# Kernel optimization log

Measured on AMD Instinct MI355X. Metric: run time of the kernel, lower is better.

The kernel has to match this reference:

```python
import jax, jax.numpy as jnp
import numpy as np

H = 50  # hidden_size


def _lstm_layer(x_seq, W_ih, W_hh, b):
    """Single-layer LSTM over a full sequence.
    x_seq: [B, T, D]; W_ih: [4H, D]; W_hh: [4H, H]; b: [4H] (b_ih + b_hh).
    Gate order matches PyTorch: i, f, g, o. Returns hidden seq [B, T, H].
    """
    B = x_seq.shape[0]
    # Precompute the input projection for every timestep in one GEMM.
    xW = jnp.einsum('btd,gd->btg', x_seq, W_ih) + b          # [B, T, 4H]
    xW = jnp.swapaxes(xW, 0, 1)                              # [T, B, 4H] time-major for scan

    def step(carry, xg):
        h, c = carry
        gates = xg + h @ W_hh.T                              # [B, 4H]
        i, f, g, o = jnp.split(gates, 4, axis=-1)
        i = jax.nn.sigmoid(i)
        f = jax.nn.sigmoid(f)
        g = jnp.tanh(g)
        o = jax.nn.sigmoid(o)
        c = f * c + i * g
        h = o * jnp.tanh(c)
        return (h, c), h

    init = (jnp.zeros((B, H), x_seq.dtype), jnp.zeros((B, H), x_seq.dtype))
    _, hs = jax.lax.scan(step, init, xW)                     # hs: [T, B, H]
    return jnp.swapaxes(hs, 0, 1)                            # [B, T, H]


def setup_inputs() -> dict:
    key = jax.random.key(0)
    ks = jax.random.split(key, 9)
    B, T, D, O = 4096, 512, 2, 1
    s = 1.0 / np.sqrt(H)  # PyTorch LSTM init scale: U(-1/sqrt(H), 1/sqrt(H))
    u = lambda k, shape: jax.random.uniform(k, shape, jnp.float32, -s, s)
    return {
        'x': jax.random.normal(ks[0], (B, T, D), jnp.float32),
        'W_ih0': u(ks[1], (4 * H, D)),
        'W_hh0': u(ks[2], (4 * H, H)),
        'b0': u(ks[3], (4 * H,)),   # b_ih + b_hh folded into one bias (identical math)
        'W_ih1': u(ks[4], (4 * H, H)),
        'W_hh1': u(ks[5], (4 * H, H)),
        'b1': u(ks[6], (4 * H,)),
        'W_fc': u(ks[7], (O, H)),
        'b_fc': u(ks[8], (O,)),
    }


def reference(x, W_ih0, W_hh0, b0, W_ih1, W_hh1, b1, W_fc, b_fc):
    h0 = _lstm_layer(x, W_ih0, W_hh0, b0)    # [B, T, H] layer 0
    h1 = _lstm_layer(h0, W_ih1, W_hh1, b1)   # [B, T, H] layer 1
    # Final-step linear head: out = fc(out[:, -1, :])
    return h1[:, -1, :] @ W_fc.T + b_fc      # [B, 1]
```

## Files before the change

### kernel.cpp

```cpp
#include <hip/hip_runtime.h>


typedef _Float16 f16;
typedef f16  f16x8 __attribute__((ext_vector_type(8)));
typedef float f32x4 __attribute__((ext_vector_type(4)));
typedef unsigned short u16;
typedef unsigned int   u32;

#define TT   512
#define MB   16
#define KP   136
#define XTP  513
#define BLK  512

__device__ __forceinline__ float sigm(float x) {
    return __builtin_amdgcn_rcpf(1.0f + __expf(-x));
}
__device__ __forceinline__ float tanh_(float x) {
    return 1.0f - 2.0f * __builtin_amdgcn_rcpf(__expf(2.0f * x) + 1.0f);
}

__device__ __forceinline__ float welem(int layer, int g, int u, int k,
        const float* __restrict__ Wih0, const float* __restrict__ Whh0,
        const float* __restrict__ b0,
        const float* __restrict__ Wih1, const float* __restrict__ Whh1,
        const float* __restrict__ b1) {
    if (u >= 50) return 0.0f;
    const int row = g * 50 + u;
    if (layer == 0) {
        if (k < 50)  return Whh0[row * 50 + k];
        if (k < 52)  return Wih0[row * 2 + (k - 50)];
        if (k == 52) return b0[row];
        return 0.0f;
    } else {
        if (k < 50)             return Wih1[row * 50 + k];
        if (k == 52)            return b1[row];
        if (k >= 64 && k < 114) return Whh1[row * 50 + (k - 64)];
        return 0.0f;
    }
}

extern "C" __global__ void __launch_bounds__(BLK, 2)
lstm2_mfma8(const float* __restrict__ x,
            const float* __restrict__ W_ih0, const float* __restrict__ W_hh0,
            const float* __restrict__ b0,
            const float* __restrict__ W_ih1, const float* __restrict__ W_hh1,
            const float* __restrict__ b1,
            const float* __restrict__ W_fc,  const float* __restrict__ b_fc,
            float* __restrict__ out)
{
    __shared__ __align__(16) u16 hc[2][MB][KP];
    __shared__ u32  xpack[MB][XTP];
    __shared__ float hfin[MB][52];

    const int tid   = threadIdx.x;
    const int lane  = tid & 63;
    const int wid   = tid >> 6;
    const int layer = wid >> 2;
    const int ub    = wid & 3;
    const int col   = lane & 15;
    const int kg    = lane >> 4;
    const int bbase = blockIdx.x * MB;

    for (int idx = tid; idx < MB * TT; idx += BLK) {
        const int b = idx >> 9, t = idx & (TT - 1);
        const float2 v = *reinterpret_cast<const float2*>(
            x + ((size_t)(bbase + b) * TT + t) * 2);
        xpack[b][t] = (u32)__builtin_bit_cast(u16, (f16)v.x)
                    | ((u32)__builtin_bit_cast(u16, (f16)v.y) << 16);
    }
    {
        u32* hcU = reinterpret_cast<u32*>(&hc[0][0][0]);
        for (int i = tid; i < 2 * MB * KP / 2; i += BLK) hcU[i] = 0;
    }
    __syncthreads();
    if (tid < 32) hc[tid >> 4][tid & 15][52] = (u16)0x3C00;
    else if (tid < 48)
        *reinterpret_cast<u32*>(&hc[0][tid - 32][50]) = xpack[tid - 32][0];

    const int u = 16 * ub + col;
    f16x8 bf[4][4];
#pragma unroll
    for (int g = 0; g < 4; ++g) {
#pragma unroll
        for (int kf = 0; kf < 4; ++kf) {
            f16x8 v;
#pragma unroll
            for (int e = 0; e < 8; ++e)
                v[e] = (f16)welem(layer, g, u, kf * 32 + 8 * kg + e,
                                  W_ih0, W_hh0, b0, W_ih1, W_hh1, b1);
            bf[g][kf] = v;
        }
    }

    float cst[4] = {0.f, 0.f, 0.f, 0.f};
    __syncthreads();

    for (int it = 0; it <= TT; ++it) {
        const int p = it & 1, q = p ^ 1;

        f16x8 a[4];
#pragma unroll
        for (int kf = 0; kf < 4; ++kf)
            a[kf] = *reinterpret_cast<const f16x8*>(&hc[p][col][kf * 32 + 8 * kg]);

        f32x4 acc[4];
        const f32x4 z = {0.f, 0.f, 0.f, 0.f};
        if (layer == 0) {
#pragma unroll
            for (int g = 0; g < 4; ++g) {
                f32x4 c = __builtin_amdgcn_mfma_f32_16x16x32_f16(a[0], bf[g][0], z, 0, 0, 0);
                acc[g]  = __builtin_amdgcn_mfma_f32_16x16x32_f16(a[1], bf[g][1], c, 0, 0, 0);
            }
        } else {
#pragma unroll
            for (int g = 0; g < 4; ++g) {
                f32x4 c = __builtin_amdgcn_mfma_f32_16x16x32_f16(a[0], bf[g][0], z, 0, 0, 0);
                c       = __builtin_amdgcn_mfma_f32_16x16x32_f16(a[1], bf[g][1], c, 0, 0, 0);
                c       = __builtin_amdgcn_mfma_f32_16x16x32_f16(a[2], bf[g][2], c, 0, 0, 0);
                acc[g]  = __builtin_amdgcn_mfma_f32_16x16x32_f16(a[3], bf[g][3], c, 0, 0, 0);
            }
        }

        const bool ew = (layer == 0) ? (it < TT) : (it >= 1);
        if (ew && u < 50) {
#pragma unroll
            for (int r = 0; r < 4; ++r) {
                const int bat = 4 * kg + r;
                const float ig = sigm (acc[0][r]);
                const float fg = sigm (acc[1][r]);
                const float gg = tanh_(acc[2][r]);
                const float og = sigm (acc[3][r]);
                cst[r] = fmaf(fg, cst[r], ig * gg);
                const float h = og * tanh_(cst[r]);
                hc[q][bat][(layer ? 64 : 0) + u] = __builtin_bit_cast(u16, (f16)h);
                if (layer == 1 && it == TT) hfin[bat][u] = h;
            }
        }
        if (wid == 0 && lane < MB && (it + 1) < TT)
            *reinterpret_cast<u32*>(&hc[q][lane][50]) = xpack[lane][it + 1];

        __syncthreads();
    }

    if (tid < MB) {
        float d = b_fc[0];
#pragma unroll
        for (int uu = 0; uu < 50; ++uu) d = fmaf(W_fc[uu], hfin[tid][uu], d);
        out[bbase + tid] = d;
    }
}

extern "C" void kernel_launch(void* const* d_in, const int* in_sizes, int n_in,
                              void* d_out, int out_size, void* d_ws, size_t ws_size,
                              hipStream_t stream) {
    const float* x     = (const float*)d_in[0];
    const float* W_ih0 = (const float*)d_in[1];
    const float* W_hh0 = (const float*)d_in[2];
    const float* b0    = (const float*)d_in[3];
    const float* W_ih1 = (const float*)d_in[4];
    const float* W_hh1 = (const float*)d_in[5];
    const float* b1    = (const float*)d_in[6];
    const float* W_fc  = (const float*)d_in[7];
    const float* b_fc  = (const float*)d_in[8];
    float* out = (float*)d_out;

    const int B = in_sizes[0] / (TT * 2);
    dim3 grid(B / MB), block(BLK);
    hipLaunchKernelGGL(lstm2_mfma8, grid, block, 0, stream,
                       x, W_ih0, W_hh0, b0, W_ih1, W_hh1, b1, W_fc, b_fc, out);
}
```

Before: 398.8 us.

## Double waves per block to split elementwise gates; fold exp scaling into weights

The block grows to 1024 threads, so each layer now has 8 waves. Wave pairs run the same MFMA gate product redundantly, and each wave handles only half of the four batch rows in the elementwise LSTM update. This halves the serial transcendental work per wave on the recurrence critical path. The -log2e and 2·log2e scale factors are folded into the fp16 weights and bias so the gates use exp2 directly without a multiply. The costs are that MFMA work is duplicated, occupancy drops to one block per CU, and the fp16 weights carry scaled values with slightly different rounding.

```diff
diff --git a/kernel.cpp b/kernel.cpp
--- a/kernel.cpp
+++ b/kernel.cpp
@@ -11,14 +11,17 @@
 #define MB   16
 #define KP   136
 #define XTP  513
-#define BLK  512
+#define BLK  1024
 
-__device__ __forceinline__ float sigm(float x) {
-    return __builtin_amdgcn_rcpf(1.0f + __expf(-x));
-}
-__device__ __forceinline__ float tanh_(float x) {
-    return 1.0f - 2.0f * __builtin_amdgcn_rcpf(__expf(2.0f * x) + 1.0f);
-}
+#if __has_builtin(__builtin_amdgcn_exp2f)
+#define EXP2(v) __builtin_amdgcn_exp2f(v)
+#else
+#define EXP2(v) __expf((v) * 0.6931471805599453f)
+#endif
+__device__ __forceinline__ float rcp_(float v) { return __builtin_amdgcn_rcpf(v); }
+
+#define L2E  1.4426950408889634f
+#define L2E2 2.8853900817779268f
 
 __device__ __forceinline__ float welem(int layer, int g, int u, int k,
         const float* __restrict__ Wih0, const float* __restrict__ Whh0,
@@ -26,28 +29,29 @@
         const float* __restrict__ Wih1, const float* __restrict__ Whh1,
         const float* __restrict__ b1) {
     if (u >= 50) return 0.0f;
+    const float s = (g == 2) ? L2E2 : -L2E;
     const int row = g * 50 + u;
     if (layer == 0) {
-        if (k < 50)  return Whh0[row * 50 + k];
-        if (k < 52)  return Wih0[row * 2 + (k - 50)];
-        if (k == 52) return b0[row];
+        if (k < 50)  return s * Whh0[row * 50 + k];
+        if (k < 52)  return s * Wih0[row * 2 + (k - 50)];
+        if (k == 52) return s * b0[row];
         return 0.0f;
     } else {
-        if (k < 50)             return Wih1[row * 50 + k];
-        if (k == 52)            return b1[row];
-        if (k >= 64 && k < 114) return Whh1[row * 50 + (k - 64)];
+        if (k < 50)             return s * Wih1[row * 50 + k];
+        if (k == 52)            return s * b1[row];
+        if (k >= 64 && k < 114) return s * Whh1[row * 50 + (k - 64)];
         return 0.0f;
     }
 }
 
-extern "C" __global__ void __launch_bounds__(BLK, 2)
-lstm2_mfma8(const float* __restrict__ x,
-            const float* __restrict__ W_ih0, const float* __restrict__ W_hh0,
-            const float* __restrict__ b0,
-            const float* __restrict__ W_ih1, const float* __restrict__ W_hh1,
-            const float* __restrict__ b1,
-            const float* __restrict__ W_fc,  const float* __restrict__ b_fc,
-            float* __restrict__ out)
+extern "C" __global__ void __launch_bounds__(BLK, 1)
+lstm2_mfma16(const float* __restrict__ x,
+             const float* __restrict__ W_ih0, const float* __restrict__ W_hh0,
+             const float* __restrict__ b0,
+             const float* __restrict__ W_ih1, const float* __restrict__ W_hh1,
+             const float* __restrict__ b1,
+             const float* __restrict__ W_fc,  const float* __restrict__ b_fc,
+             float* __restrict__ out)
 {
     __shared__ __align__(16) u16 hc[2][MB][KP];
     __shared__ u32  xpack[MB][XTP];
@@ -56,7 +60,8 @@
     const int tid   = threadIdx.x;
     const int lane  = tid & 63;
     const int wid   = tid >> 6;
-    const int layer = wid >> 2;
+    const int layer = wid >> 3;
+    const int sub   = (wid >> 2) & 1;
     const int ub    = wid & 3;
     const int col   = lane & 15;
     const int kg    = lane >> 4;
@@ -93,7 +98,8 @@
         }
     }
 
-    float cst[4] = {0.f, 0.f, 0.f, 0.f};
+    float c0 = 0.0f, c1 = 0.0f;
+    const int hbase = layer ? 64 : 0;
     __syncthreads();
 
     for (int it = 0; it <= TT; ++it) {
@@ -122,21 +128,29 @@
             }
         }
 
+#define EWBODY(R, CS)                                                         \
+        {                                                                     \
+            const int bat = 4 * kg + (R);                                     \
+            const float eI = EXP2(acc[0][R]);                                 \
+            const float eF = EXP2(acc[1][R]);                                 \
+            const float eG = EXP2(acc[2][R]);                                 \
+            const float eO = EXP2(acc[3][R]);                                 \
+            const float ig = rcp_(1.0f + eI);                                 \
+            const float fg = rcp_(1.0f + eF);                                 \
+            const float gg = fmaf(-2.0f, rcp_(1.0f + eG), 1.0f);              \
+            const float og = rcp_(1.0f + eO);                                 \
+            CS = fmaf(fg, CS, ig * gg);                                       \
+            const float eC = EXP2(CS * L2E2);                                 \
+            const float h  = og * fmaf(-2.0f, rcp_(1.0f + eC), 1.0f);         \
+            hc[q][bat][hbase + u] = __builtin_bit_cast(u16, (f16)h);          \
+            if (layer == 1 && it == TT) hfin[bat][u] = h;                     \
+        }
         const bool ew = (layer == 0) ? (it < TT) : (it >= 1);
         if (ew && u < 50) {
-#pragma unroll
-            for (int r = 0; r < 4; ++r) {
-                const int bat = 4 * kg + r;
-                const float ig = sigm (acc[0][r]);
-                const float fg = sigm (acc[1][r]);
-                const float gg = tanh_(acc[2][r]);
-                const float og = sigm (acc[3][r]);
-                cst[r] = fmaf(fg, cst[r], ig * gg);
-                const float h = og * tanh_(cst[r]);
-                hc[q][bat][(layer ? 64 : 0) + u] = __builtin_bit_cast(u16, (f16)h);
-                if (layer == 1 && it == TT) hfin[bat][u] = h;
-            }
+            if (sub == 0) { EWBODY(0, c0) EWBODY(1, c1) }
+            else          { EWBODY(2, c0) EWBODY(3, c1) }
         }
+#undef EWBODY
         if (wid == 0 && lane < MB && (it + 1) < TT)
             *reinterpret_cast<u32*>(&hc[q][lane][50]) = xpack[lane][it + 1];
 
@@ -167,6 +181,6 @@
 
     const int B = in_sizes[0] / (TT * 2);
     dim3 grid(B / MB), block(BLK);
-    hipLaunchKernelGGL(lstm2_mfma8, grid, block, 0, stream,
+    hipLaunchKernelGGL(lstm2_mfma16, grid, block, 0, stream,
                        x, W_ih0, W_hh0, b0, W_ih1, W_hh1, b1, W_fc, b_fc, out);
 }
```

Result: slower. 1.184 ms (+197.0%).

## Decouple LSTM layers with LDS counter handshakes and fold exp scaling into weights

Applied to the files above, without the earlier changes.

Replaces the per-timestep block-wide barrier with LDS atomic counters, so the layer-0 waves run ahead of the layer-1 waves through a 4-slot ring of hidden states. Layer 1 keeps its own double buffer. The log2(e) factors are folded into the weights so the gate activations can use exp2 and merged reciprocals. MFMA sections are given raised wave priority. The aim is to take the barrier stall off the serial critical path and trim transcendental work, at the cost of spin-wait polling and reliance on correct LDS memory ordering.

```diff
diff --git a/kernel.cpp b/kernel.cpp
--- a/kernel.cpp
+++ b/kernel.cpp
@@ -9,16 +9,15 @@
 
 #define TT   512
 #define MB   16
-#define KP   136
+#define RK   72
 #define XTP  513
 #define BLK  512
 
-__device__ __forceinline__ float sigm(float x) {
-    return __builtin_amdgcn_rcpf(1.0f + __expf(-x));
-}
-__device__ __forceinline__ float tanh_(float x) {
-    return 1.0f - 2.0f * __builtin_amdgcn_rcpf(__expf(2.0f * x) + 1.0f);
-}
+#define EXP2(v) __builtin_amdgcn_exp2f(v)
+__device__ __forceinline__ float rcp_(float v) { return __builtin_amdgcn_rcpf(v); }
+
+#define L2E  1.4426950408889634f
+#define L2E2 2.8853900817779268f
 
 __device__ __forceinline__ float welem(int layer, int g, int u, int k,
         const float* __restrict__ Wih0, const float* __restrict__ Whh0,
@@ -26,22 +25,38 @@
         const float* __restrict__ Wih1, const float* __restrict__ Whh1,
         const float* __restrict__ b1) {
     if (u >= 50) return 0.0f;
+    const float s = (g == 2) ? L2E2 : -L2E;
     const int row = g * 50 + u;
     if (layer == 0) {
-        if (k < 50)  return Whh0[row * 50 + k];
-        if (k < 52)  return Wih0[row * 2 + (k - 50)];
-        if (k == 52) return b0[row];
+        if (k < 50)  return s * Whh0[row * 50 + k];
+        if (k < 52)  return s * Wih0[row * 2 + (k - 50)];
+        if (k == 52) return s * b0[row];
         return 0.0f;
     } else {
-        if (k < 50)             return Wih1[row * 50 + k];
-        if (k == 52)            return b1[row];
-        if (k >= 64 && k < 114) return Whh1[row * 50 + (k - 64)];
+        if (k < 50)             return s * Wih1[row * 50 + k];
+        if (k == 52)            return s * b1[row];
+        if (k >= 64 && k < 114) return s * Whh1[row * 50 + (k - 64)];
         return 0.0f;
     }
 }
 
+#define EWFUSED(YI, YF, YG, YO, CS, HOUT)                                     \
+    {                                                                         \
+        const float eI = EXP2(YI);                                            \
+        const float eF = EXP2(YF);                                            \
+        const float eG = EXP2(YG);                                            \
+        const float eO = EXP2(YO);                                            \
+        const float fg  = rcp_(1.0f + eF);                                    \
+        const float num = fmaf(L2E2, eG, -L2E2);                              \
+        const float igg = num * rcp_((1.0f + eI) * (1.0f + eG));              \
+        CS = fmaf(fg, CS, igg);                                               \
+        const float cc = fminf(fmaxf(CS, -80.0f), 80.0f);                     \
+        const float eC = EXP2(cc);                                            \
+        HOUT = (eC - 1.0f) * rcp_((1.0f + eO) * (eC + 1.0f));                 \
+    }
+
 extern "C" __global__ void __launch_bounds__(BLK, 2)
-lstm2_mfma8(const float* __restrict__ x,
+lstm2_async(const float* __restrict__ x,
             const float* __restrict__ W_ih0, const float* __restrict__ W_hh0,
             const float* __restrict__ b0,
             const float* __restrict__ W_ih1, const float* __restrict__ W_hh1,
@@ -49,9 +64,11 @@
             const float* __restrict__ W_fc,  const float* __restrict__ b_fc,
             float* __restrict__ out)
 {
-    __shared__ __align__(16) u16 hc[2][MB][KP];
-    __shared__ u32  xpack[MB][XTP];
+    __shared__ __align__(16) u16 ring[4][MB][RK];
+    __shared__ __align__(16) u16 h1b[2][MB][RK];
+    __shared__ u32   xpack[MB][XTP];
     __shared__ float hfin[MB][52];
+    __shared__ u32   ctr0, ctr1;
 
     const int tid   = threadIdx.x;
     const int lane  = tid & 63;
@@ -70,13 +87,16 @@
                     | ((u32)__builtin_bit_cast(u16, (f16)v.y) << 16);
     }
     {
-        u32* hcU = reinterpret_cast<u32*>(&hc[0][0][0]);
-        for (int i = tid; i < 2 * MB * KP / 2; i += BLK) hcU[i] = 0;
-    }
+        u32* p = reinterpret_cast<u32*>(&ring[0][0][0]);
+        for (int i = tid; i < (int)(sizeof(ring) / 4); i += BLK) p[i] = 0;
+        u32* q = reinterpret_cast<u32*>(&h1b[0][0][0]);
+        for (int i = tid; i < (int)(sizeof(h1b) / 4); i += BLK) q[i] = 0;
+    }
+    if (tid == 0) { ctr0 = 0; ctr1 = 0; }
     __syncthreads();
-    if (tid < 32) hc[tid >> 4][tid & 15][52] = (u16)0x3C00;
-    else if (tid < 48)
-        *reinterpret_cast<u32*>(&hc[0][tid - 32][50]) = xpack[tid - 32][0];
+    if (tid < 64) ring[tid >> 4][tid & 15][52] = (u16)0x3C00;
+    else if (tid < 80)
+        *reinterpret_cast<u32*>(&ring[3][tid - 64][50]) = xpack[tid - 64][0];
 
     const int u = 16 * ub + col;
     f16x8 bf[4][4];
@@ -93,61 +113,93 @@
         }
     }
 
+    __syncthreads();
+
+    volatile u32* vc0 = &ctr0;
+    volatile u32* vc1 = &ctr1;
     float cst[4] = {0.f, 0.f, 0.f, 0.f};
-    __syncthreads();
-
-    for (int it = 0; it <= TT; ++it) {
-        const int p = it & 1, q = p ^ 1;
-
-        f16x8 a[4];
-#pragma unroll
-        for (int kf = 0; kf < 4; ++kf)
-            a[kf] = *reinterpret_cast<const f16x8*>(&hc[p][col][kf * 32 + 8 * kg]);
-
-        f32x4 acc[4];
-        const f32x4 z = {0.f, 0.f, 0.f, 0.f};
-        if (layer == 0) {
+    const f32x4 z = {0.f, 0.f, 0.f, 0.f};
+
+    if (layer == 0) {
+        for (int s = 0; s < TT; ++s) {
+            while (*vc0 < (u32)(4 * s)) __builtin_amdgcn_s_sleep(1);
+            const int rs = (s + 3) & 3, ws = s & 3;
+            const f16x8 a0 = *reinterpret_cast<const f16x8*>(&ring[rs][col][8 * kg]);
+            const f16x8 a1 = *reinterpret_cast<const f16x8*>(&ring[rs][col][32 + 8 * kg]);
+            f32x4 acc[4];
+            __builtin_amdgcn_s_setprio(1);
 #pragma unroll
             for (int g = 0; g < 4; ++g) {
-                f32x4 c = __builtin_amdgcn_mfma_f32_16x16x32_f16(a[0], bf[g][0], z, 0, 0, 0);
-                acc[g]  = __builtin_amdgcn_mfma_f32_16x16x32_f16(a[1], bf[g][1], c, 0, 0, 0);
-            }
-        } else {
+                f32x4 c = __builtin_amdgcn_mfma_f32_16x16x32_f16(a0, bf[g][0], z, 0, 0, 0);
+                acc[g]  = __builtin_amdgcn_mfma_f32_16x16x32_f16(a1, bf[g][1], c, 0, 0, 0);
+            }
+            __builtin_amdgcn_s_setprio(0);
+            u16 hw[4];
+#pragma unroll
+            for (int r = 0; r < 4; ++r) {
+                float hv;
+                EWFUSED(acc[0][r], acc[1][r], acc[2][r], acc[3][r], cst[r], hv);
+                hw[r] = __builtin_bit_cast(u16, (f16)hv);
+            }
+            if (s >= 4)
+                while (*vc1 < (u32)(4 * (s - 3))) __builtin_amdgcn_s_sleep(1);
+            if (u < 50) {
+#pragma unroll
+                for (int r = 0; r < 4; ++r) ring[ws][4 * kg + r][u] = hw[r];
+            }
+            if (wid == 0 && lane < MB && (s + 1) < TT)
+                *reinterpret_cast<u32*>(&ring[ws][lane][50]) = xpack[lane][s + 1];
+            __threadfence_block();
+            if (lane == 0) atomicAdd(&ctr0, 1u);
+        }
+    } else {
+        for (int t = 0; t < TT; ++t) {
+            while (*vc0 < (u32)(4 * (t + 1))) __builtin_amdgcn_s_sleep(1);
+            while (*vc1 < (u32)(4 * t))       __builtin_amdgcn_s_sleep(1);
+            const int rs = t & 3, wb = t & 1, rb = wb ^ 1;
+            const f16x8 a0 = *reinterpret_cast<const f16x8*>(&ring[rs][col][8 * kg]);
+            const f16x8 a1 = *reinterpret_cast<const f16x8*>(&ring[rs][col][32 + 8 * kg]);
+            const f16x8 a2 = *reinterpret_cast<const f16x8*>(&h1b[rb][col][8 * kg]);
+            const f16x8 a3 = *reinterpret_cast<const f16x8*>(&h1b[rb][col][32 + 8 * kg]);
+            f32x4 acc[4];
+            __builtin_amdgcn_s_setprio(1);
 #pragma unroll
             for (int g = 0; g < 4; ++g) {
-                f32x4 c = __builtin_amdgcn_mfma_f32_16x16x32_f16(a[0], bf[g][0], z, 0, 0, 0);
-                c       = __builtin_amdgcn_mfma_f32_16x16x32_f16(a[1], bf[g][1], c, 0, 0, 0);
-                c       = __builtin_amdgcn_mfma_f32_16x16x32_f16(a[2], bf[g][2], c, 0, 0, 0);
-                acc[g]  = __builtin_amdgcn_mfma_f32_16x16x32_f16(a[3], bf[g][3], c, 0, 0, 0);
-            }
-        }
-
-        const bool ew = (layer == 0) ? (it < TT) : (it >= 1);
-        if (ew && u < 50) {
+                f32x4 c = __builtin_amdgcn_mfma_f32_16x16x32_f16(a0, bf[g][0], z, 0, 0, 0);
+                c       = __builtin_amdgcn_mfma_f32_16x16x32_f16(a1, bf[g][1], c, 0, 0, 0);
+                c       = __builtin_amdgcn_mfma_f32_16x16x32_f16(a2, bf[g][2], c, 0, 0, 0);
+                acc[g]  = __builtin_amdgcn_mfma_f32_16x16x32_f16(a3, bf[g][3], c, 0, 0, 0);
+            }
+            __builtin_amdgcn_s_setprio(0);
+            u16 hw[4]; float hf[4];
 #pragma unroll
             for (int r = 0; r < 4; ++r) {
-                const int bat = 4 * kg + r;
-                const float ig = sigm (acc[0][r]);
-                const float fg = sigm (acc[1][r]);
-                const float gg = tanh_(acc[2][r]);
-                const float og = sigm (acc[3][r]);
-                cst[r] = fmaf(fg, cst[r], ig * gg);
-                const float h = og * tanh_(cst[r]);
-                hc[q][bat][(layer ? 64 : 0) + u] = __builtin_bit_cast(u16, (f16)h);
-                if (layer == 1 && it == TT) hfin[bat][u] = h;
-            }
-        }
-        if (wid == 0 && lane < MB && (it + 1) < TT)
-            *reinterpret_cast<u32*>(&hc[q][lane][50]) = xpack[lane][it + 1];
-
-        __syncthreads();
-    }
-
-    if (tid < MB) {
-        float d = b_fc[0];
-#pragma unroll
-        for (int uu = 0; uu < 50; ++uu) d = fmaf(W_fc[uu], hfin[tid][uu], d);
-        out[bbase + tid] = d;
+                float hv;
+                EWFUSED(acc[0][r], acc[1][r], acc[2][r], acc[3][r], cst[r], hv);
+                hw[r] = __builtin_bit_cast(u16, (f16)hv);
+                hf[r] = hv;
+            }
+            if (u < 50) {
+#pragma unroll
+                for (int r = 0; r < 4; ++r) h1b[wb][4 * kg + r][u] = hw[r];
+                if (t == TT - 1) {
+#pragma unroll
+                    for (int r = 0; r < 4; ++r) hfin[4 * kg + r][u] = hf[r];
+                }
+            }
+            __threadfence_block();
+            if (lane == 0) atomicAdd(&ctr1, 1u);
+        }
+        if (wid == 4) {
+            while (*vc1 < (u32)(4 * TT)) __builtin_amdgcn_s_sleep(1);
+            if (lane < MB) {
+                float d = b_fc[0];
+#pragma unroll
+                for (int uu = 0; uu < 50; ++uu)
+                    d = fmaf(W_fc[uu], hfin[lane][uu], d);
+                out[bbase + lane] = d;
+            }
+        }
     }
 }
 
@@ -167,6 +219,6 @@
 
     const int B = in_sizes[0] / (TT * 2);
     dim3 grid(B / MB), block(BLK);
-    hipLaunchKernelGGL(lstm2_mfma8, grid, block, 0, stream,
+    hipLaunchKernelGGL(lstm2_async, grid, block, 0, stream,
                        x, W_ih0, W_hh0, b0, W_ih1, W_hh1, b1, W_fc, b_fc, out);
 }
```

Measured after the change: 399.8 us, median of 2. No clear change (+0.3%).
